# Kernel optimization log

Measured on AMD Instinct MI355X. Metric: run time of the kernel, lower is better.

Reference implementation:

```python
import jax, jax.numpy as jnp
import numpy as np

D_MODEL = 1024
NUM_HEADS = 16
D_K = D_MODEL // NUM_HEADS
D_FF = 4096


def setup_inputs() -> dict:
    key = jax.random.key(0)
    ks = jax.random.split(key, 12)
    s = 1.0 / np.sqrt(D_MODEL)
    sf = 1.0 / np.sqrt(D_FF)
    return {
        "x": jax.random.normal(ks[0], (2, 2048, D_MODEL), dtype=jnp.float32),
        # nn.Linear weights are [out_features, in_features]
        "Wq": jax.random.uniform(ks[1], (D_MODEL, D_MODEL), jnp.float32, -s, s),
        "Wk": jax.random.uniform(ks[2], (D_MODEL, D_MODEL), jnp.float32, -s, s),
        "Wv": jax.random.uniform(ks[3], (D_MODEL, D_MODEL), jnp.float32, -s, s),
        "Wo": jax.random.uniform(ks[4], (D_MODEL, D_MODEL), jnp.float32, -s, s),
        "W1": jax.random.uniform(ks[5], (D_FF, D_MODEL), jnp.float32, -s, s),
        "W2": jax.random.uniform(ks[6], (D_MODEL, D_FF), jnp.float32, -sf, sf),
        "g1": jnp.ones((D_MODEL,), jnp.float32),
        "b1": jnp.zeros((D_MODEL,), jnp.float32),
        "g2": jnp.ones((D_MODEL,), jnp.float32),
        "b2": jnp.zeros((D_MODEL,), jnp.float32),
    }


def _layer_norm(x, gamma, beta, eps=1e-5):
    mu = jnp.mean(x, axis=-1, keepdims=True)
    var = jnp.mean((x - mu) ** 2, axis=-1, keepdims=True)
    return (x - mu) * jax.lax.rsqrt(var + eps) * gamma + beta


def reference(x, Wq, Wk, Wv, Wo, W1, W2, g1, b1, g2, b2):
    B, S, _ = x.shape
    H, Dk = NUM_HEADS, D_K
    # projections (Linear: x @ W.T), split heads -> [B, H, S, Dk]
    q = (x @ Wq.T).reshape(B, S, H, Dk).transpose(0, 2, 1, 3)
    k = (x @ Wk.T).reshape(B, S, H, Dk).transpose(0, 2, 1, 3)
    v = (x @ Wv.T).reshape(B, S, H, Dk).transpose(0, 2, 1, 3)
    scores = jnp.einsum('bhsd,bhtd->bhst', q, k) / jnp.sqrt(jnp.float32(Dk))
    attn = jax.nn.softmax(scores, axis=-1)
    out = jnp.einsum('bhst,bhtd->bhsd', attn, v)
    out = out.transpose(0, 2, 1, 3).reshape(B, S, H * Dk)
    out = out @ Wo.T
    x_after_attn = _layer_norm(x + out, g1, b1)
    ff = jax.nn.gelu(x_after_attn @ W1.T, approximate=False)
    ff_out = ff @ W2.T
    return _layer_norm(x_after_attn + ff_out, g2, b2)
```

## Files before the change

kernel.cpp:

```cpp
#include <hip/hip_runtime.h>
#include <hip/hip_bf16.h>
#include <cstdint>
#include <cstddef>

#define D_MODEL 1024
#define D_FF    4096
#define NTOK    4096
#define SEQ     2048
#define NH      16
#define DK      64
#define LDQ     3072

typedef __bf16 bf16;
typedef __bf16 bf16_8 __attribute__((ext_vector_type(8)));
typedef __bf16 bf16_4 __attribute__((ext_vector_type(4)));
typedef float  f32_4  __attribute__((ext_vector_type(4)));

__device__ __forceinline__ void async_copy16(const bf16* g, bf16* l) {
    __builtin_amdgcn_global_load_lds((const __attribute__((address_space(1))) void*)g,
                                     (__attribute__((address_space(3))) void*)l,
                                     16, 0, 0);
}

__global__ __launch_bounds__(256)
void cast_all(const float* __restrict__ x,  const float* __restrict__ Wq,
              const float* __restrict__ Wk, const float* __restrict__ Wv,
              const float* __restrict__ Wo, const float* __restrict__ W1,
              const float* __restrict__ W2,
              bf16* __restrict__ xb, bf16* __restrict__ Wqkvb,
              bf16* __restrict__ Wob, bf16* __restrict__ W1b,
              bf16* __restrict__ W2b) {
    const int blk = blockIdx.x;
    const float* s; bf16* d; int off;
    if (blk < 4096)       { s = x;  d = xb;              off = blk; }
    else if (blk < 5120)  { s = Wq; d = Wqkvb;           off = blk - 4096; }
    else if (blk < 6144)  { s = Wk; d = Wqkvb + 1048576; off = blk - 5120; }
    else if (blk < 7168)  { s = Wv; d = Wqkvb + 2097152; off = blk - 6144; }
    else if (blk < 8192)  { s = Wo; d = Wob;             off = blk - 7168; }
    else if (blk < 12288) { s = W1; d = W1b;             off = blk - 8192; }
    else                  { s = W2; d = W2b;             off = blk - 12288; }
    const int i = off * 1024 + threadIdx.x * 4;
    float4 v = *(const float4*)(s + i);
    bf16_4 o;
    o[0] = (bf16)v.x; o[1] = (bf16)v.y; o[2] = (bf16)v.z; o[3] = (bf16)v.w;
    *(bf16_4*)(d + i) = o;
}

template <int EPI>
__global__ __launch_bounds__(256, 2)
void gemm_bt(const bf16* __restrict__ A, const bf16* __restrict__ B,
             bf16* __restrict__ C0, size_t cstride, bf16* __restrict__ Vt,
             int M, int N, int ldk, int kLen) {
    __shared__ bf16 As[128 * 64];
    __shared__ bf16 Bs[128 * 64];
    const int tid  = threadIdx.x;
    const int wave = tid >> 6, lane = tid & 63;
    const int quad = lane >> 4, l15 = lane & 15;
    const int wm = wave >> 1, wn = wave & 1;
    const int bm = blockIdx.x, bn = blockIdx.y, z = blockIdx.z;

    const bf16* A0 = A + (size_t)bm * 128 * ldk + (size_t)z * kLen;
    const bf16* B0 = B + (size_t)bn * 128 * ldk + (size_t)z * kLen;

    f32_4 acc[4][4];
#pragma unroll
    for (int i = 0; i < 4; i++)
#pragma unroll
        for (int j = 0; j < 4; j++) acc[i][j] = (f32_4){0.f, 0.f, 0.f, 0.f};

    const int srow8 = lane >> 3;
    const int slog  = (lane & 7) ^ srow8;
    const int rx    = l15 & 7;

    for (int k0 = 0; k0 < kLen; k0 += 64) {
#pragma unroll
        for (int c = 0; c < 4; c++) {
            int row = c * 32 + wave * 8 + srow8;
            async_copy16(&A0[(size_t)row * ldk + k0 + slog * 8],
                         &As[(c * 32 + wave * 8) * 64]);
        }
#pragma unroll
        for (int c = 0; c < 4; c++) {
            int row = c * 32 + wave * 8 + srow8;
            async_copy16(&B0[(size_t)row * ldk + k0 + slog * 8],
                         &Bs[(c * 32 + wave * 8) * 64]);
        }
        __syncthreads();

#pragma unroll
        for (int kh = 0; kh < 2; kh++) {
            bf16_8 af[4], bfr[4];
#pragma unroll
            for (int mi = 0; mi < 4; mi++)
                af[mi] = *(const bf16_8*)&As[(wm * 64 + mi * 16 + l15) * 64 +
                                             (((kh * 4 + quad) ^ rx) * 8)];
#pragma unroll
            for (int ni = 0; ni < 4; ni++)
                bfr[ni] = *(const bf16_8*)&Bs[(wn * 64 + ni * 16 + l15) * 64 +
                                              (((kh * 4 + quad) ^ rx) * 8)];
#pragma unroll
            for (int mi = 0; mi < 4; mi++)
#pragma unroll
                for (int ni = 0; ni < 4; ni++)
                    acc[mi][ni] = __builtin_amdgcn_mfma_f32_16x16x32_bf16(
                        af[mi], bfr[ni], acc[mi][ni], 0, 0, 0);
        }
        __syncthreads();
    }

    bf16* C = C0 + (size_t)z * cstride;
    const int row0 = bm * 128 + wm * 64 + quad * 4;
    const int col0 = bn * 128 + wn * 64 + l15;

    if (EPI == 3 && bn >= 16) {
        const int bvt = bm >> 4;
#pragma unroll
        for (int mi = 0; mi < 4; mi++) {
            const int srow = (row0 + mi * 16) & 2047;
#pragma unroll
            for (int ni = 0; ni < 4; ni++) {
                const int ch = col0 + ni * 16 - 2048;
                bf16_4 w;
#pragma unroll
                for (int r = 0; r < 4; r++) w[r] = (bf16)acc[mi][ni][r];
                *(bf16_4*)&Vt[((size_t)(bvt * 1024 + ch)) * SEQ + srow] = w;
            }
        }
        return;
    }

#pragma unroll
    for (int mi = 0; mi < 4; mi++) {
#pragma unroll
        for (int ni = 0; ni < 4; ni++) {
#pragma unroll
            for (int r = 0; r < 4; r++) {
                int row = row0 + mi * 16 + r;
                int col = col0 + ni * 16;
                size_t idx = (size_t)row * N + col;
                float v = acc[mi][ni][r];
                if (EPI == 2) {
                    float g = 0.5f * v * (1.0f + erff(v * 0.70710678118654752f));
                    C[idx] = (bf16)g;
                } else {
                    C[idx] = (bf16)v;
                }
            }
        }
    }
}

__global__ __launch_bounds__(256)
void attn3(const bf16* __restrict__ QKV, const bf16* __restrict__ Vt,
           bf16* __restrict__ O) {
    __shared__ bf16 Ks[64 * 64];
    __shared__ bf16 Vs[64 * 64];
    __shared__ bf16 Ps[4][16 * 80];

    const int tid  = threadIdx.x;
    const int wave = tid >> 6, lane = tid & 63;
    const int quad = lane >> 4, l15 = lane & 15;
    const int qb = blockIdx.x & 31;
    const int h  = (blockIdx.x >> 5) & 15;
    const int b  = blockIdx.x >> 9;

    const bf16* Qg = QKV + (size_t)(b * SEQ) * LDQ + h * 64;
    const bf16* Kg = QKV + (size_t)(b * SEQ) * LDQ + 1024 + h * 64;
    const bf16* Vg = Vt + (size_t)(b * 1024 + h * 64) * SEQ;

    const int qrow = qb * 64 + wave * 16 + l15;
    const bf16_8 qf0 = *(const bf16_8*)&Qg[(size_t)qrow * LDQ + quad * 8];
    const bf16_8 qf1 = *(const bf16_8*)&Qg[(size_t)qrow * LDQ + 32 + quad * 8];

    const int srow = wave * 8 + (lane >> 3);
    const int sg   = lane & 7;
    const int xl   = l15 & 7;

    float l_lane = 0.f;
    f32_4 o_acc[4];
#pragma unroll
    for (int d = 0; d < 4; d++) o_acc[d] = (f32_4){0.f, 0.f, 0.f, 0.f};

    bf16* P = Ps[wave];

    for (int t = 0; t < SEQ / 64; ++t) {
        const int k0 = t * 64;
        __syncthreads();
#pragma unroll
        for (int c = 0; c < 2; ++c) {
            int r = c * 32 + srow;
            async_copy16(&Kg[(size_t)(k0 + r) * LDQ + ((sg ^ (r & 7)) * 8)],
                         &Ks[c * 2048 + wave * 512]);
            async_copy16(&Vg[(size_t)r * SEQ + k0 + ((sg ^ (r & 7)) * 8)],
                         &Vs[c * 2048 + wave * 512]);
        }
        __syncthreads();

        f32_4 s[4];
#pragma unroll
        for (int ni = 0; ni < 4; ni++) {
            const bf16* kp = &Ks[(ni * 16 + l15) * 64];
            bf16_8 kb0 = *(const bf16_8*)&kp[(quad ^ xl) * 8];
            bf16_8 kb1 = *(const bf16_8*)&kp[((quad + 4) ^ xl) * 8];
            f32_4 z = (f32_4){0.f, 0.f, 0.f, 0.f};
            z = __builtin_amdgcn_mfma_f32_16x16x32_bf16(kb0, qf0, z, 0, 0, 0);
            s[ni] = __builtin_amdgcn_mfma_f32_16x16x32_bf16(kb1, qf1, z, 0, 0, 0);
        }

#pragma unroll
        for (int ni = 0; ni < 4; ni++) {
            bf16_4 pk;
#pragma unroll
            for (int r = 0; r < 4; r++) {
                float p = __expf(fmaf(s[ni][r], 0.125f, -8.0f));
                l_lane += p;
                pk[r] = (bf16)p;
            }
            int G = ni * 2 + (quad >> 1);
            *(bf16_4*)&P[l15 * 80 + ((G ^ xl) * 8) + ((quad & 1) * 4)] = pk;
        }
        bf16_8 pf0 = *(const bf16_8*)&P[l15 * 80 + ((quad ^ xl) * 8)];
        bf16_8 pf1 = *(const bf16_8*)&P[l15 * 80 + (((quad + 4) ^ xl) * 8)];

#pragma unroll
        for (int dt = 0; dt < 4; dt++) {
            const bf16* vp = &Vs[(dt * 16 + l15) * 64];
            bf16_8 vb0 = *(const bf16_8*)&vp[(quad ^ xl) * 8];
            bf16_8 vb1 = *(const bf16_8*)&vp[((quad + 4) ^ xl) * 8];
            o_acc[dt] = __builtin_amdgcn_mfma_f32_16x16x32_bf16(vb0, pf0, o_acc[dt], 0, 0, 0);
            o_acc[dt] = __builtin_amdgcn_mfma_f32_16x16x32_bf16(vb1, pf1, o_acc[dt], 0, 0, 0);
        }
    }

    l_lane += __shfl_xor(l_lane, 16);
    l_lane += __shfl_xor(l_lane, 32);
    const float rl = 1.0f / l_lane;

#pragma unroll
    for (int dt = 0; dt < 4; dt++) {
        bf16_4 pk;
#pragma unroll
        for (int r = 0; r < 4; r++) pk[r] = (bf16)(o_acc[dt][r] * rl);
        int G = dt * 2 + (quad >> 1);
        *(bf16_4*)&P[l15 * 80 + ((G ^ xl) * 8) + ((quad & 1) * 4)] = pk;
    }
    const int q2 = lane >> 2, dc = lane & 3, x2 = q2 & 7;
    bf16_8 o0 = *(const bf16_8*)&P[q2 * 80 + (((dc * 2) ^ x2) * 8)];
    bf16_8 o1 = *(const bf16_8*)&P[q2 * 80 + (((dc * 2 + 1) ^ x2) * 8)];
    const size_t row = (size_t)b * SEQ + qb * 64 + wave * 16 + q2;
    *(bf16_8*)&O[row * D_MODEL + h * 64 + dc * 16] = o0;
    *(bf16_8*)&O[row * D_MODEL + h * 64 + dc * 16 + 8] = o1;
}

template <bool A32, bool O32>
__global__ __launch_bounds__(256)
void ln_kernel(const void* __restrict__ av, const bf16* __restrict__ p0,
               const bf16* __restrict__ p1, const bf16* __restrict__ p2,
               const bf16* __restrict__ p3,
               const float* __restrict__ gamma, const float* __restrict__ beta,
               void* __restrict__ yv) {
    const int row = blockIdx.x;
    const int tid = threadIdx.x;
    const size_t off = (size_t)row * D_MODEL;
    float v[4];
    {
        bf16_4 a0 = *(const bf16_4*)(p0 + off + tid * 4);
        bf16_4 a1 = *(const bf16_4*)(p1 + off + tid * 4);
        bf16_4 a2 = *(const bf16_4*)(p2 + off + tid * 4);
        bf16_4 a3 = *(const bf16_4*)(p3 + off + tid * 4);
        if (A32) {
            float4 xa = *(const float4*)((const float*)av + off + tid * 4);
            v[0] = xa.x; v[1] = xa.y; v[2] = xa.z; v[3] = xa.w;
        } else {
            bf16_4 xa = *(const bf16_4*)((const bf16*)av + off + tid * 4);
#pragma unroll
            for (int i = 0; i < 4; i++) v[i] = (float)xa[i];
        }
#pragma unroll
        for (int i = 0; i < 4; i++)
            v[i] += ((float)a0[i] + (float)a1[i]) + ((float)a2[i] + (float)a3[i]);
    }
    float s = v[0] + v[1] + v[2] + v[3];
    float ss = v[0] * v[0] + v[1] * v[1] + v[2] * v[2] + v[3] * v[3];
#pragma unroll
    for (int m = 1; m < 64; m <<= 1) {
        s  += __shfl_xor(s, m);
        ss += __shfl_xor(ss, m);
    }
    __shared__ float red_s[4], red_q[4];
    int wave = tid >> 6, lane = tid & 63;
    if (lane == 0) { red_s[wave] = s; red_q[wave] = ss; }
    __syncthreads();
    s  = red_s[0] + red_s[1] + red_s[2] + red_s[3];
    ss = red_q[0] + red_q[1] + red_q[2] + red_q[3];
    float mu   = s * (1.f / D_MODEL);
    float var  = ss * (1.f / D_MODEL) - mu * mu;
    float rstd = rsqrtf(var + 1e-5f);
    float4 gg = *(const float4*)(gamma + tid * 4);
    float4 be = *(const float4*)(beta + tid * 4);
    float y0 = (v[0] - mu) * rstd * gg.x + be.x;
    float y1 = (v[1] - mu) * rstd * gg.y + be.y;
    float y2 = (v[2] - mu) * rstd * gg.z + be.z;
    float y3 = (v[3] - mu) * rstd * gg.w + be.w;
    if (O32) {
        *(float4*)((float*)yv + off + tid * 4) = make_float4(y0, y1, y2, y3);
    } else {
        bf16_4 o;
        o[0] = (bf16)y0; o[1] = (bf16)y1; o[2] = (bf16)y2; o[3] = (bf16)y3;
        *(bf16_4*)((bf16*)yv + off + tid * 4) = o;
    }
}

extern "C" void kernel_launch(void* const* d_in, const int* in_sizes, int n_in,
                              void* d_out, int out_size, void* d_ws, size_t ws_size,
                              hipStream_t stream) {
    (void)in_sizes; (void)n_in; (void)out_size; (void)ws_size;
    const float* x  = (const float*)d_in[0];
    const float* Wq = (const float*)d_in[1];
    const float* Wk = (const float*)d_in[2];
    const float* Wv = (const float*)d_in[3];
    const float* Wo = (const float*)d_in[4];
    const float* W1 = (const float*)d_in[5];
    const float* W2 = (const float*)d_in[6];
    const float* g1 = (const float*)d_in[7];
    const float* b1 = (const float*)d_in[8];
    const float* g2 = (const float*)d_in[9];
    const float* b2 = (const float*)d_in[10];

    char* ws = (char*)d_ws;
    bf16*  xb    = (bf16*)(ws + 0);
    bf16*  aob   = xb;
    bf16*  ln1b  = (bf16*)(ws + 0);
    bf16*  QKVb  = (bf16*)(ws + 8388608);
    bf16*  Vtb   = (bf16*)(ws + 33554432);
    bf16*  hb    = (bf16*)(ws + 8388608);
    bf16*  Wqkvb = (bf16*)(ws + 41943040);
    bf16*  Wob   = (bf16*)(ws + 48234496);
    bf16*  W1b   = (bf16*)(ws + 50331648);
    bf16*  W2b   = (bf16*)(ws + 58720256);
    bf16*  proj0 = (bf16*)(ws + 67108864);
    const size_t PSTRIDE = (size_t)NTOK * D_MODEL;

    cast_all<<<dim3(16384), 256, 0, stream>>>(x, Wq, Wk, Wv, Wo, W1, W2,
                                              xb, Wqkvb, Wob, W1b, W2b);

    gemm_bt<3><<<dim3(NTOK / 128, 3072 / 128, 1), 256, 0, stream>>>(
        xb, Wqkvb, QKVb, 0, Vtb, NTOK, 3072, D_MODEL, D_MODEL);

    attn3<<<dim3(1024), 256, 0, stream>>>(QKVb, Vtb, aob);

    gemm_bt<0><<<dim3(NTOK / 128, D_MODEL / 128, 4), 256, 0, stream>>>(
        aob, Wob, proj0, PSTRIDE, nullptr, NTOK, D_MODEL, D_MODEL, 256);
    ln_kernel<true, false><<<NTOK, 256, 0, stream>>>(
        x, proj0, proj0 + PSTRIDE, proj0 + 2 * PSTRIDE, proj0 + 3 * PSTRIDE,
        g1, b1, ln1b);

    gemm_bt<2><<<dim3(NTOK / 128, D_FF / 128, 1), 256, 0, stream>>>(
        ln1b, W1b, hb, 0, nullptr, NTOK, D_FF, D_MODEL, D_MODEL);

    gemm_bt<0><<<dim3(NTOK / 128, D_MODEL / 128, 4), 256, 0, stream>>>(
        hb, W2b, proj0, PSTRIDE, nullptr, NTOK, D_MODEL, D_FF, 1024);
    ln_kernel<false, true><<<NTOK, 256, 0, stream>>>(
        ln1b, proj0, proj0 + PSTRIDE, proj0 + 2 * PSTRIDE, proj0 + 3 * PSTRIDE,
        g2, b2, d_out);
}
```

Before: 332.3 us.

## Double-buffer K/V tiles and keep attention probabilities in registers

The attention kernel now double-buffers K and V in shared memory, prefetching the next 64-key tile with async copies while the current tile is computed, so each iteration needs one barrier instead of two. The P matrix no longer round-trips through shared memory: K rows are loaded in a permuted order so the score MFMA output lands directly in the B-operand layout for the PV MFMA. The row-sum is kept as a vector accumulator. This doubles K/V LDS use and relies on the row permutation being correct.

```diff
diff --git a/kernel.cpp b/kernel.cpp
--- a/kernel.cpp
+++ b/kernel.cpp
@@ -151,11 +151,10 @@
 }
 
 __global__ __launch_bounds__(256)
-void attn3(const bf16* __restrict__ QKV, const bf16* __restrict__ Vt,
+void attn4(const bf16* __restrict__ QKV, const bf16* __restrict__ Vt,
            bf16* __restrict__ O) {
-    __shared__ bf16 Ks[64 * 64];
-    __shared__ bf16 Vs[64 * 64];
-    __shared__ bf16 Ps[4][16 * 80];
+    __shared__ bf16 Ks[2][64 * 64];
+    __shared__ bf16 Vs[2][64 * 64];
 
     const int tid  = threadIdx.x;
     const int wave = tid >> 6, lane = tid & 63;
@@ -172,34 +171,48 @@
     const bf16_8 qf0 = *(const bf16_8*)&Qg[(size_t)qrow * LDQ + quad * 8];
     const bf16_8 qf1 = *(const bf16_8*)&Qg[(size_t)qrow * LDQ + 32 + quad * 8];
 
-    const int srow = wave * 8 + (lane >> 3);
-    const int sg   = lane & 7;
-    const int xl   = l15 & 7;
-
-    float l_lane = 0.f;
+    const int m0 = wave * 8 + (lane >> 3);
+    const int sg = lane & 7;
+    const int sw = m0 & 7;
+    const int xl = l15 & 7;
+    const int fr = ((m0 >> 4) << 5) | ((m0 & 12) << 1) | (m0 & 3);
+
+    f32_4 lac = (f32_4){0.f, 0.f, 0.f, 0.f};
     f32_4 o_acc[4];
 #pragma unroll
     for (int d = 0; d < 4; d++) o_acc[d] = (f32_4){0.f, 0.f, 0.f, 0.f};
 
-    bf16* P = Ps[wave];
+    async_copy16(&Kg[(size_t)fr * LDQ + ((sg ^ sw) * 8)], &Ks[0][wave * 512]);
+    async_copy16(&Kg[(size_t)(fr + 4) * LDQ + ((sg ^ sw) * 8)],
+                 &Ks[0][2048 + wave * 512]);
+    async_copy16(&Vg[(size_t)m0 * SEQ + ((sg ^ sw) * 8)], &Vs[0][wave * 512]);
+    async_copy16(&Vg[(size_t)(m0 + 32) * SEQ + ((sg ^ sw) * 8)],
+                 &Vs[0][2048 + wave * 512]);
+    __syncthreads();
 
     for (int t = 0; t < SEQ / 64; ++t) {
-        const int k0 = t * 64;
-        __syncthreads();
-#pragma unroll
-        for (int c = 0; c < 2; ++c) {
-            int r = c * 32 + srow;
-            async_copy16(&Kg[(size_t)(k0 + r) * LDQ + ((sg ^ (r & 7)) * 8)],
-                         &Ks[c * 2048 + wave * 512]);
-            async_copy16(&Vg[(size_t)r * SEQ + k0 + ((sg ^ (r & 7)) * 8)],
-                         &Vs[c * 2048 + wave * 512]);
-        }
-        __syncthreads();
+        const int cur = t & 1;
+        if (t + 1 < SEQ / 64) {
+            const int k1 = (t + 1) * 64;
+            bf16* kd = Ks[cur ^ 1];
+            bf16* vd = Vs[cur ^ 1];
+            async_copy16(&Kg[(size_t)(k1 + fr) * LDQ + ((sg ^ sw) * 8)],
+                         kd + wave * 512);
+            async_copy16(&Kg[(size_t)(k1 + fr + 4) * LDQ + ((sg ^ sw) * 8)],
+                         kd + 2048 + wave * 512);
+            async_copy16(&Vg[(size_t)m0 * SEQ + k1 + ((sg ^ sw) * 8)],
+                         vd + wave * 512);
+            async_copy16(&Vg[(size_t)(m0 + 32) * SEQ + k1 + ((sg ^ sw) * 8)],
+                         vd + 2048 + wave * 512);
+        }
+
+        const bf16* KsC = Ks[cur];
+        const bf16* VsC = Vs[cur];
 
         f32_4 s[4];
 #pragma unroll
         for (int ni = 0; ni < 4; ni++) {
-            const bf16* kp = &Ks[(ni * 16 + l15) * 64];
+            const bf16* kp = &KsC[(ni * 16 + l15) * 64];
             bf16_8 kb0 = *(const bf16_8*)&kp[(quad ^ xl) * 8];
             bf16_8 kb1 = *(const bf16_8*)&kp[((quad + 4) ^ xl) * 8];
             f32_4 z = (f32_4){0.f, 0.f, 0.f, 0.f};
@@ -207,35 +220,38 @@
             s[ni] = __builtin_amdgcn_mfma_f32_16x16x32_bf16(kb1, qf1, z, 0, 0, 0);
         }
 
+        bf16_8 pf0, pf1;
 #pragma unroll
         for (int ni = 0; ni < 4; ni++) {
-            bf16_4 pk;
 #pragma unroll
             for (int r = 0; r < 4; r++) {
                 float p = __expf(fmaf(s[ni][r], 0.125f, -8.0f));
-                l_lane += p;
-                pk[r] = (bf16)p;
+                lac[r] += p;
+                bf16 pb = (bf16)p;
+                const int j = ((ni >> 1) << 2) + r;
+                if ((ni & 1) == 0) pf0[j] = pb;
+                else               pf1[j] = pb;
             }
-            int G = ni * 2 + (quad >> 1);
-            *(bf16_4*)&P[l15 * 80 + ((G ^ xl) * 8) + ((quad & 1) * 4)] = pk;
-        }
-        bf16_8 pf0 = *(const bf16_8*)&P[l15 * 80 + ((quad ^ xl) * 8)];
-        bf16_8 pf1 = *(const bf16_8*)&P[l15 * 80 + (((quad + 4) ^ xl) * 8)];
+        }
 
 #pragma unroll
         for (int dt = 0; dt < 4; dt++) {
-            const bf16* vp = &Vs[(dt * 16 + l15) * 64];
+            const bf16* vp = &VsC[(dt * 16 + l15) * 64];
             bf16_8 vb0 = *(const bf16_8*)&vp[(quad ^ xl) * 8];
             bf16_8 vb1 = *(const bf16_8*)&vp[((quad + 4) ^ xl) * 8];
             o_acc[dt] = __builtin_amdgcn_mfma_f32_16x16x32_bf16(vb0, pf0, o_acc[dt], 0, 0, 0);
             o_acc[dt] = __builtin_amdgcn_mfma_f32_16x16x32_bf16(vb1, pf1, o_acc[dt], 0, 0, 0);
         }
-    }
-
+
+        __syncthreads();
+    }
+
+    float l_lane = (lac[0] + lac[1]) + (lac[2] + lac[3]);
     l_lane += __shfl_xor(l_lane, 16);
     l_lane += __shfl_xor(l_lane, 32);
     const float rl = 1.0f / l_lane;
 
+    bf16* P = (bf16*)Ks + wave * 1280;
 #pragma unroll
     for (int dt = 0; dt < 4; dt++) {
         bf16_4 pk;
@@ -347,7 +363,7 @@
     gemm_bt<3><<<dim3(NTOK / 128, 3072 / 128, 1), 256, 0, stream>>>(
         xb, Wqkvb, QKVb, 0, Vtb, NTOK, 3072, D_MODEL, D_MODEL);
 
-    attn3<<<dim3(1024), 256, 0, stream>>>(QKVb, Vtb, aob);
+    attn4<<<dim3(1024), 256, 0, stream>>>(QKVb, Vtb, aob);
 
     gemm_bt<0><<<dim3(NTOK / 128, D_MODEL / 128, 4), 256, 0, stream>>>(
         aob, Wob, proj0, PSTRIDE, nullptr, NTOK, D_MODEL, D_MODEL, 256);
```

Measured after the change: 327.0 us. About the same (-1.6%).
